# Kernel tuning notes

Measured on AMD Instinct MI355X. Metric: run time of the kernel, lower is better.

Reference implementation:

```python
import jax, jax.numpy as jnp
import numpy as np

A = 100.0
EPSILON = 0.1
NUM_NEG = 10
N = 100000
DIM = 64


def setup_inputs() -> dict:
    key = jax.random.key(0)
    k1, k2, k3 = jax.random.split(key, 3)
    x = jax.random.normal(k1, (N, DIM), dtype=jnp.float32)
    u_idx = jax.random.randint(k2, (N * NUM_NEG,), 0, N)
    v_idx = jax.random.randint(k3, (N * NUM_NEG,), 0, N)
    return {"x": x, "u_idx": u_idx, "v_idx": v_idx}


def reference(x, u_idx, v_idx):
    # Minkowski signature vector J = [-1, 1, ..., 1]
    J = jnp.ones((DIM,), dtype=x.dtype).at[0].set(-1.0)

    xu = x[u_idx]                      # (E, dim) gather
    xv = x[v_idx]                      # (E, dim) gather

    inner = jnp.sum(xu * xv * J, axis=-1)                 # (E,) Minkowski inner product
    inner = jnp.minimum(inner, -1.0 - 1e-7)               # clamp(max=-1-1e-7)
    dist = jnp.arccosh(-inner)                            # hyperbolic distance

    mask = dist < EPSILON                                 # data-dependent activity mask
    delta = jnp.where(mask, EPSILON - dist, 0.0)          # zero out inactive pairs

    energy = 0.5 * A * jnp.sum(delta ** 2) / NUM_NEG

    denom = jnp.sqrt(inner ** 2 - 1.0)
    force_mag = A * delta / NUM_NEG                       # already zero where inactive
    factor = jnp.where(mask, -(force_mag / (denom + 1e-9)), 0.0)[:, None]  # (E,1)

    grad = jnp.zeros_like(x)
    grad = grad.at[u_idx].add(factor * (xv * J))          # scatter-add over pairs
    grad = grad.at[v_idx].add(factor * (xu * J))
    return energy, grad
```

## Files before the change

### kernel.cpp

```cpp
#include <hip/hip_runtime.h>

#define EPS_F 0.1f
#define A_F 100.0f
#define NUMNEG_F 10.0f
#define EXP_EPS 1.1051709f
#define CAP 64
#define BATCH 16
#define NBLOCKS 4096

__global__ __launch_bounds__(256) void fill_kernel(
    const int* __restrict__ u_idx, const int* __restrict__ v_idx,
    int* __restrict__ counts, int* __restrict__ entries,
    float* __restrict__ out, int out_n, int E)
{
    const int tid = blockIdx.x * blockDim.x + threadIdx.x;
    const int nthreads = gridDim.x * blockDim.x;

    float4* o4 = (float4*)out;
    const int n4 = out_n >> 2;
    for (int i = tid; i < n4; i += nthreads) o4[i] = float4{0.f, 0.f, 0.f, 0.f};
    if (tid == 0)
        for (int i = n4 * 4; i < out_n; i++) out[i] = 0.f;

    for (int i = tid; i < E; i += nthreads) {
        const int u = u_idx[i];
        const int slot = atomicAdd(&counts[u], 1);
        if (slot < CAP) entries[u * CAP + slot] = v_idx[i];
    }
}

__global__ __launch_bounds__(256) void node_kernel(
    const float* __restrict__ x,
    const int* __restrict__ counts,
    const int* __restrict__ entries,
    float* __restrict__ out,
    float* __restrict__ block_energy,
    int N)
{
    const int lane = threadIdx.x & 63;
    const int wib  = threadIdx.x >> 6;
    const int wave = (blockIdx.x * blockDim.x + threadIdx.x) >> 6;
    const int nwaves = (gridDim.x * blockDim.x) >> 6;
    const float sign = (lane == 0) ? -1.0f : 1.0f;
    float* __restrict__ grad = out + 1;

    float eacc = 0.0f;

    int u = wave;
    int deg = 0, myv = 0;
    if (u < N) {
        deg = counts[u];
        myv = entries[u * CAP + lane];
    }

    while (u < N) {
        const int deg_c = min(deg, CAP);
        const int myv_c = myv;
        const float xu = x[(size_t)u * 64 + lane];

        const int un = u + nwaves;
        if (un < N) {
            deg = counts[un];
            myv = entries[un * CAP + lane];
        }

        float gacc = 0.0f;
        for (int k0 = 0; k0 < deg_c; k0 += BATCH) {
            const int bn = min(BATCH, deg_c - k0);
            int vs[BATCH]; float xv[BATCH], p[BATCH];

            #pragma unroll
            for (int k = 0; k < BATCH; k++) {
                if (k < bn) {
                    vs[k] = __builtin_amdgcn_readlane(myv_c, k0 + k);
                    xv[k] = x[(size_t)vs[k] * 64 + lane];
                }
            }
            #pragma unroll
            for (int k = 0; k < BATCH; k++)
                p[k] = (k < bn) ? xu * xv[k] * sign : 0.0f;

            #pragma unroll
            for (int off = 32; off >= 1; off >>= 1) {
                #pragma unroll
                for (int k = 0; k < BATCH; k++)
                    if (k < bn) p[k] += __shfl_xor(p[k], off, 64);
            }

            #pragma unroll
            for (int k = 0; k < BATCH; k++) {
                if (k < bn) {
                    const float inner = fminf(p[k], -1.0f - 1e-7f);
                    const float s = sqrtf(inner * inner - 1.0f);
                    const float t = -inner + s;
                    if (t < EXP_EPS) {
                        const float dist = __logf(t);
                        const float delta = EPS_F - dist;
                        eacc += delta * delta;
                        const float factor = -(A_F / NUMNEG_F) * delta / (s + 1e-9f);
                        unsafeAtomicAdd(&grad[(size_t)vs[k] * 64 + lane],
                                        factor * xu * sign);
                        gacc = fmaf(factor, xv[k], gacc);
                    }
                }
            }
        }
        if (deg_c > 0)
            unsafeAtomicAdd(&grad[(size_t)u * 64 + lane], gacc * sign);
        u = un;
    }

    __shared__ float se[4];
    if (lane == 0) se[wib] = eacc;
    __syncthreads();
    if (threadIdx.x == 0)
        block_energy[blockIdx.x] = se[0] + se[1] + se[2] + se[3];
}

__global__ __launch_bounds__(256) void energy_reduce_kernel(
    const float* __restrict__ block_energy, float* __restrict__ out, int n)
{
    const int lane = threadIdx.x & 63;
    const int wib  = threadIdx.x >> 6;
    float s = 0.0f;
    for (int i = threadIdx.x; i < n; i += 256) s += block_energy[i];
    #pragma unroll
    for (int off = 32; off >= 1; off >>= 1) s += __shfl_xor(s, off, 64);
    __shared__ float se[4];
    if (lane == 0) se[wib] = s;
    __syncthreads();
    if (threadIdx.x == 0)
        out[0] = (se[0] + se[1] + se[2] + se[3]) * (0.5f * A_F / NUMNEG_F);
}

extern "C" void kernel_launch(void* const* d_in, const int* in_sizes, int n_in,
                              void* d_out, int out_size, void* d_ws, size_t ws_size,
                              hipStream_t stream) {
    const float* x     = (const float*)d_in[0];
    const int*   u_idx = (const int*)d_in[1];
    const int*   v_idx = (const int*)d_in[2];
    float* out = (float*)d_out;
    const int E = in_sizes[1];
    const int N = in_sizes[0] / 64;

    char* ws = (char*)d_ws;
    int*   counts       = (int*)ws;
    int*   entries      = (int*)(ws + (1 << 20));
    float* block_energy = (float*)(ws + (1 << 20) + (size_t)N * CAP * 4 + (1 << 20));

    hipMemsetAsync(counts, 0, (size_t)N * sizeof(int), stream);

    fill_kernel<<<4096, 256, 0, stream>>>(u_idx, v_idx, counts, entries,
                                          out, out_size, E);

    node_kernel<<<NBLOCKS, 256, 0, stream>>>(x, counts, entries, out, block_energy, N);

    energy_reduce_kernel<<<1, 256, 0, stream>>>(block_energy, out, NBLOCKS);
}
```

Baseline: 332.1 us.

## Replace node bucketing with direct per-edge processing and transposed batched reduction

```diff
diff --git a/kernel.cpp b/kernel.cpp
--- a/kernel.cpp
+++ b/kernel.cpp
@@ -4,38 +4,22 @@
 #define A_F 100.0f
 #define NUMNEG_F 10.0f
 #define EXP_EPS 1.1051709f
-#define CAP 64
 #define BATCH 16
 #define NBLOCKS 4096
 
-__global__ __launch_bounds__(256) void fill_kernel(
-    const int* __restrict__ u_idx, const int* __restrict__ v_idx,
-    int* __restrict__ counts, int* __restrict__ entries,
-    float* __restrict__ out, int out_n, int E)
-{
-    const int tid = blockIdx.x * blockDim.x + threadIdx.x;
-    const int nthreads = gridDim.x * blockDim.x;
-
-    float4* o4 = (float4*)out;
-    const int n4 = out_n >> 2;
-    for (int i = tid; i < n4; i += nthreads) o4[i] = float4{0.f, 0.f, 0.f, 0.f};
-    if (tid == 0)
-        for (int i = n4 * 4; i < out_n; i++) out[i] = 0.f;
-
-    for (int i = tid; i < E; i += nthreads) {
-        const int u = u_idx[i];
-        const int slot = atomicAdd(&counts[u], 1);
-        if (slot < CAP) entries[u * CAP + slot] = v_idx[i];
-    }
+__device__ __forceinline__ float red2(float a, float b, int dist, bool sel) {
+    const float fa = a + __shfl_xor(a, dist, 64);
+    const float fb = b + __shfl_xor(b, dist, 64);
+    return sel ? fb : fa;
 }
 
-__global__ __launch_bounds__(256) void node_kernel(
+__global__ __launch_bounds__(256) void edge_kernel(
     const float* __restrict__ x,
-    const int* __restrict__ counts,
-    const int* __restrict__ entries,
+    const int* __restrict__ u_idx,
+    const int* __restrict__ v_idx,
     float* __restrict__ out,
     float* __restrict__ block_energy,
-    int N)
+    int E)
 {
     const int lane = threadIdx.x & 63;
     const int wib  = threadIdx.x >> 6;
@@ -44,74 +28,80 @@
     const float sign = (lane == 0) ? -1.0f : 1.0f;
     float* __restrict__ grad = out + 1;
 
+    const bool m32 = (lane & 32) != 0;
+    const bool m16 = (lane & 16) != 0;
+    const bool m8  = (lane & 8)  != 0;
+    const bool m4  = (lane & 4)  != 0;
+    const int  e4  = (lane >> 2) & 15;
+
     float eacc = 0.0f;
 
-    int u = wave;
-    int deg = 0, myv = 0;
-    if (u < N) {
-        deg = counts[u];
-        myv = entries[u * CAP + lane];
+    for (int base = wave * BATCH; base < E; base += nwaves * BATCH) {
+        const int bn = min(BATCH, E - base);
+
+        int uu = 0, vv = 0;
+        if (lane < bn) { uu = u_idx[base + lane]; vv = v_idx[base + lane]; }
+
+        int us[BATCH], vs[BATCH];
+        float xuj[BATCH], xv[BATCH];
+        #pragma unroll
+        for (int k = 0; k < BATCH; k++) {
+            if (k < bn) {
+                us[k]  = __builtin_amdgcn_readlane(uu, k);
+                vs[k]  = __builtin_amdgcn_readlane(vv, k);
+                xuj[k] = x[(size_t)us[k] * 64 + lane] * sign;
+                xv[k]  = x[(size_t)vs[k] * 64 + lane];
+            } else { us[k] = 0; vs[k] = 0; xuj[k] = 0.0f; xv[k] = 0.0f; }
+        }
+
+        float p[BATCH];
+        #pragma unroll
+        for (int k = 0; k < BATCH; k++) p[k] = xuj[k] * xv[k];
+
+        float q0 = red2(p[0], p[8],  32, m32);
+        float q1 = red2(p[1], p[9],  32, m32);
+        float q2 = red2(p[2], p[10], 32, m32);
+        float q3 = red2(p[3], p[11], 32, m32);
+        float q4 = red2(p[4], p[12], 32, m32);
+        float q5 = red2(p[5], p[13], 32, m32);
+        float q6 = red2(p[6], p[14], 32, m32);
+        float q7 = red2(p[7], p[15], 32, m32);
+        float r0 = red2(q0, q4, 16, m16);
+        float r1 = red2(q1, q5, 16, m16);
+        float r2 = red2(q2, q6, 16, m16);
+        float r3 = red2(q3, q7, 16, m16);
+        float s0 = red2(r0, r2, 8, m8);
+        float s1 = red2(r1, r3, 8, m8);
+        float t0 = red2(s0, s1, 4, m4);
+        t0 += __shfl_xor(t0, 2, 64);
+        t0 += __shfl_xor(t0, 1, 64);
+
+        const float inner = fminf(t0, -1.0f - 1e-7f);
+        const float s     = __builtin_amdgcn_sqrtf(fmaf(inner, inner, -1.0f));
+        const float t     = s - inner;
+        const bool  act   = (t < EXP_EPS) & (e4 < bn);
+        const float dist  = __logf(t);
+        const float delta = act ? (EPS_F - dist) : 0.0f;
+        eacc = fmaf(delta, delta, eacc);
+        const float factor = (-(A_F / NUMNEG_F)) * delta *
+                             __builtin_amdgcn_rcpf(s + 1e-9f);
+
+        const unsigned long long ball = __ballot(act);
+        #pragma unroll
+        for (int k = 0; k < BATCH; k++) {
+            if ((ball >> (4 * k)) & 1ull) {
+                const float fk = __uint_as_float(
+                    __builtin_amdgcn_readlane(__float_as_uint(factor), 4 * k));
+                unsafeAtomicAdd(&grad[(size_t)vs[k] * 64 + lane], fk * xuj[k]);
+                unsafeAtomicAdd(&grad[(size_t)us[k] * 64 + lane], fk * xv[k] * sign);
+            }
+        }
     }
 
-    while (u < N) {
-        const int deg_c = min(deg, CAP);
-        const int myv_c = myv;
-        const float xu = x[(size_t)u * 64 + lane];
-
-        const int un = u + nwaves;
-        if (un < N) {
-            deg = counts[un];
-            myv = entries[un * CAP + lane];
-        }
-
-        float gacc = 0.0f;
-        for (int k0 = 0; k0 < deg_c; k0 += BATCH) {
-            const int bn = min(BATCH, deg_c - k0);
-            int vs[BATCH]; float xv[BATCH], p[BATCH];
-
-            #pragma unroll
-            for (int k = 0; k < BATCH; k++) {
-                if (k < bn) {
-                    vs[k] = __builtin_amdgcn_readlane(myv_c, k0 + k);
-                    xv[k] = x[(size_t)vs[k] * 64 + lane];
-                }
-            }
-            #pragma unroll
-            for (int k = 0; k < BATCH; k++)
-                p[k] = (k < bn) ? xu * xv[k] * sign : 0.0f;
-
-            #pragma unroll
-            for (int off = 32; off >= 1; off >>= 1) {
-                #pragma unroll
-                for (int k = 0; k < BATCH; k++)
-                    if (k < bn) p[k] += __shfl_xor(p[k], off, 64);
-            }
-
-            #pragma unroll
-            for (int k = 0; k < BATCH; k++) {
-                if (k < bn) {
-                    const float inner = fminf(p[k], -1.0f - 1e-7f);
-                    const float s = sqrtf(inner * inner - 1.0f);
-                    const float t = -inner + s;
-                    if (t < EXP_EPS) {
-                        const float dist = __logf(t);
-                        const float delta = EPS_F - dist;
-                        eacc += delta * delta;
-                        const float factor = -(A_F / NUMNEG_F) * delta / (s + 1e-9f);
-                        unsafeAtomicAdd(&grad[(size_t)vs[k] * 64 + lane],
-                                        factor * xu * sign);
-                        gacc = fmaf(factor, xv[k], gacc);
-                    }
-                }
-            }
-        }
-        if (deg_c > 0)
-            unsafeAtomicAdd(&grad[(size_t)u * 64 + lane], gacc * sign);
-        u = un;
-    }
-
+    #pragma unroll
+    for (int off = 32; off >= 1; off >>= 1) eacc += __shfl_xor(eacc, off, 64);
     __shared__ float se[4];
-    if (lane == 0) se[wib] = eacc;
+    if (lane == 0) se[wib] = eacc * 0.25f;
     __syncthreads();
     if (threadIdx.x == 0)
         block_energy[blockIdx.x] = se[0] + se[1] + se[2] + se[3];
@@ -141,19 +131,10 @@
     const int*   v_idx = (const int*)d_in[2];
     float* out = (float*)d_out;
     const int E = in_sizes[1];
-    const int N = in_sizes[0] / 64;
 
-    char* ws = (char*)d_ws;
-    int*   counts       = (int*)ws;
-    int*   entries      = (int*)(ws + (1 << 20));
-    float* block_energy = (float*)(ws + (1 << 20) + (size_t)N * CAP * 4 + (1 << 20));
+    float* block_energy = (float*)d_ws;
 
-    hipMemsetAsync(counts, 0, (size_t)N * sizeof(int), stream);
-
-    fill_kernel<<<4096, 256, 0, stream>>>(u_idx, v_idx, counts, entries,
-                                          out, out_size, E);
-
-    node_kernel<<<NBLOCKS, 256, 0, stream>>>(x, counts, entries, out, block_energy, N);
-
+    hipMemsetAsync(out, 0, (size_t)out_size * sizeof(float), stream);
+    edge_kernel<<<NBLOCKS, 256, 0, stream>>>(x, u_idx, v_idx, out, block_energy, E);
     energy_reduce_kernel<<<1, 256, 0, stream>>>(block_energy, out, NBLOCKS);
 }
```

New measurement: 378.4 us. 13.9% more time.

## Use transpose-style butterfly reduction for batched dot products and lane-parallel epilogue

Applied to the files above, without the earlier changes.

```diff
diff --git a/kernel.cpp b/kernel.cpp
--- a/kernel.cpp
+++ b/kernel.cpp
@@ -29,6 +29,12 @@
     }
 }
 
+__device__ __forceinline__ float red2(float a, float b, int dist, bool sel) {
+    const float fa = a + __shfl_xor(a, dist, 64);
+    const float fb = b + __shfl_xor(b, dist, 64);
+    return sel ? fb : fa;
+}
+
 __global__ __launch_bounds__(256) void node_kernel(
     const float* __restrict__ x,
     const int* __restrict__ counts,
@@ -44,6 +50,12 @@
     const float sign = (lane == 0) ? -1.0f : 1.0f;
     float* __restrict__ grad = out + 1;
 
+    const bool m32 = (lane & 32) != 0;
+    const bool m16 = (lane & 16) != 0;
+    const bool m8  = (lane & 8)  != 0;
+    const bool m4  = (lane & 4)  != 0;
+    const int  e4  = lane >> 2;
+
     float eacc = 0.0f;
 
     int u = wave;
@@ -56,7 +68,7 @@
     while (u < N) {
         const int deg_c = min(deg, CAP);
         const int myv_c = myv;
-        const float xu = x[(size_t)u * 64 + lane];
+        const float xuj = x[(size_t)u * 64 + lane] * sign;
 
         const int un = u + nwaves;
         if (un < N) {
@@ -67,41 +79,53 @@
         float gacc = 0.0f;
         for (int k0 = 0; k0 < deg_c; k0 += BATCH) {
             const int bn = min(BATCH, deg_c - k0);
+
             int vs[BATCH]; float xv[BATCH], p[BATCH];
-
             #pragma unroll
             for (int k = 0; k < BATCH; k++) {
                 if (k < bn) {
                     vs[k] = __builtin_amdgcn_readlane(myv_c, k0 + k);
                     xv[k] = x[(size_t)vs[k] * 64 + lane];
-                }
-            }
-            #pragma unroll
-            for (int k = 0; k < BATCH; k++)
-                p[k] = (k < bn) ? xu * xv[k] * sign : 0.0f;
-
-            #pragma unroll
-            for (int off = 32; off >= 1; off >>= 1) {
-                #pragma unroll
-                for (int k = 0; k < BATCH; k++)
-                    if (k < bn) p[k] += __shfl_xor(p[k], off, 64);
+                    p[k]  = xuj * xv[k];
+                } else { vs[k] = 0; xv[k] = 0.0f; p[k] = 0.0f; }
             }
 
+            float q0 = red2(p[0], p[8],  32, m32);
+            float q1 = red2(p[1], p[9],  32, m32);
+            float q2 = red2(p[2], p[10], 32, m32);
+            float q3 = red2(p[3], p[11], 32, m32);
+            float q4 = red2(p[4], p[12], 32, m32);
+            float q5 = red2(p[5], p[13], 32, m32);
+            float q6 = red2(p[6], p[14], 32, m32);
+            float q7 = red2(p[7], p[15], 32, m32);
+            float r0 = red2(q0, q4, 16, m16);
+            float r1 = red2(q1, q5, 16, m16);
+            float r2 = red2(q2, q6, 16, m16);
+            float r3 = red2(q3, q7, 16, m16);
+            float s0 = red2(r0, r2, 8, m8);
+            float s1 = red2(r1, r3, 8, m8);
+            float t0 = red2(s0, s1, 4, m4);
+            t0 += __shfl_xor(t0, 2, 64);
+            t0 += __shfl_xor(t0, 1, 64);
+
+            const float inner = fminf(t0, -1.0f - 1e-7f);
+            const float s     = __builtin_amdgcn_sqrtf(fmaf(inner, inner, -1.0f));
+            const float t     = s - inner;
+            const bool  act   = (t < EXP_EPS) & (e4 < bn);
+            const float dist  = __logf(t);
+            const float delta = act ? (EPS_F - dist) : 0.0f;
+            eacc = fmaf(delta, delta, eacc);
+            const float factor = (-(A_F / NUMNEG_F)) * delta *
+                                 __builtin_amdgcn_rcpf(s + 1e-9f);
+
+            const unsigned long long ball = __ballot(act);
             #pragma unroll
             for (int k = 0; k < BATCH; k++) {
-                if (k < bn) {
-                    const float inner = fminf(p[k], -1.0f - 1e-7f);
-                    const float s = sqrtf(inner * inner - 1.0f);
-                    const float t = -inner + s;
-                    if (t < EXP_EPS) {
-                        const float dist = __logf(t);
-                        const float delta = EPS_F - dist;
-                        eacc += delta * delta;
-                        const float factor = -(A_F / NUMNEG_F) * delta / (s + 1e-9f);
-                        unsafeAtomicAdd(&grad[(size_t)vs[k] * 64 + lane],
-                                        factor * xu * sign);
-                        gacc = fmaf(factor, xv[k], gacc);
-                    }
+                if ((ball >> (4 * k)) & 1ull) {
+                    const float fk = __uint_as_float(
+                        __builtin_amdgcn_readlane(__float_as_uint(factor), 4 * k));
+                    unsafeAtomicAdd(&grad[(size_t)vs[k] * 64 + lane], fk * xuj);
+                    gacc = fmaf(fk, xv[k], gacc);
                 }
             }
         }
@@ -110,8 +134,10 @@
         u = un;
     }
 
+    #pragma unroll
+    for (int off = 32; off >= 1; off >>= 1) eacc += __shfl_xor(eacc, off, 64);
     __shared__ float se[4];
-    if (lane == 0) se[wib] = eacc;
+    if (lane == 0) se[wib] = eacc * 0.25f;
     __syncthreads();
     if (threadIdx.x == 0)
         block_energy[blockIdx.x] = se[0] + se[1] + se[2] + se[3];
```

Result: faster. 323.5 us (-2.6%).

## Use transposed butterfly reduction and process two nodes per wave

Applied to the files above, without the earlier changes.

```diff
diff --git a/kernel.cpp b/kernel.cpp
--- a/kernel.cpp
+++ b/kernel.cpp
@@ -25,9 +25,58 @@
     for (int i = tid; i < E; i += nthreads) {
         const int u = u_idx[i];
         const int slot = atomicAdd(&counts[u], 1);
-        if (slot < CAP) entries[u * CAP + slot] = v_idx[i];
+        if (slot < CAP) entries[(size_t)u * CAP + slot] = v_idx[i];
     }
 }
+
+__device__ __forceinline__ float red2(float a, float b, int dist, bool sel) {
+    const float fa = a + __shfl_xor(a, dist, 64);
+    const float fb = b + __shfl_xor(b, dist, 64);
+    return sel ? fb : fa;
+}
+
+#define PROCESS_BATCH(xuj, vs, xv, bn, gacc)                                   \
+    do {                                                                       \
+        float p[BATCH];                                                        \
+        _Pragma("unroll")                                                      \
+        for (int k = 0; k < BATCH; k++) p[k] = (xuj) * (xv)[k];                \
+        float q0 = red2(p[0], p[8],  32, m32);                                 \
+        float q1 = red2(p[1], p[9],  32, m32);                                 \
+        float q2 = red2(p[2], p[10], 32, m32);                                 \
+        float q3 = red2(p[3], p[11], 32, m32);                                 \
+        float q4 = red2(p[4], p[12], 32, m32);                                 \
+        float q5 = red2(p[5], p[13], 32, m32);                                 \
+        float q6 = red2(p[6], p[14], 32, m32);                                 \
+        float q7 = red2(p[7], p[15], 32, m32);                                 \
+        float r0 = red2(q0, q4, 16, m16);                                      \
+        float r1 = red2(q1, q5, 16, m16);                                      \
+        float r2 = red2(q2, q6, 16, m16);                                      \
+        float r3 = red2(q3, q7, 16, m16);                                      \
+        float s0 = red2(r0, r2, 8, m8);                                        \
+        float s1 = red2(r1, r3, 8, m8);                                        \
+        float t0 = red2(s0, s1, 4, m4);                                        \
+        t0 += __shfl_xor(t0, 2, 64);                                           \
+        t0 += __shfl_xor(t0, 1, 64);                                           \
+        const float inner = fminf(t0, -1.0f - 1e-7f);                          \
+        const float sq    = __builtin_amdgcn_sqrtf(fmaf(inner, inner, -1.0f)); \
+        const float tt    = sq - inner;                                        \
+        const bool  act   = (tt < EXP_EPS) & (e4 < (bn));                      \
+        const float dist  = __logf(tt);                                        \
+        const float delta = act ? (EPS_F - dist) : 0.0f;                       \
+        eacc = fmaf(delta, delta, eacc);                                       \
+        const float factor = (-(A_F / NUMNEG_F)) * delta *                     \
+                             __builtin_amdgcn_rcpf(sq + 1e-9f);                \
+        const unsigned long long ball = __ballot(act);                         \
+        _Pragma("unroll")                                                      \
+        for (int k = 0; k < BATCH; k++) {                                      \
+            if ((ball >> (4 * k)) & 1ull) {                                    \
+                const float fk = __uint_as_float(                              \
+                    __builtin_amdgcn_readlane(__float_as_uint(factor), 4 * k));\
+                unsafeAtomicAdd(&grad[(size_t)(vs)[k] * 64 + lane], fk * (xuj));\
+                (gacc) = fmaf(fk, (xv)[k], (gacc));                            \
+            }                                                                  \
+        }                                                                      \
+    } while (0)
 
 __global__ __launch_bounds__(256) void node_kernel(
     const float* __restrict__ x,
@@ -44,74 +93,86 @@
     const float sign = (lane == 0) ? -1.0f : 1.0f;
     float* __restrict__ grad = out + 1;
 
+    const bool m32 = (lane & 32) != 0;
+    const bool m16 = (lane & 16) != 0;
+    const bool m8  = (lane & 8)  != 0;
+    const bool m4  = (lane & 4)  != 0;
+    const int  e4  = lane >> 2;
+
     float eacc = 0.0f;
 
-    int u = wave;
-    int deg = 0, myv = 0;
-    if (u < N) {
-        deg = counts[u];
-        myv = entries[u * CAP + lane];
+    int uA = wave * 2;
+    const int stride = nwaves * 2;
+    int degA = 0, myvA = 0, degB = 0, myvB = 0;
+    if (uA < N)     { degA = counts[uA];     myvA = entries[(size_t)uA * CAP + lane]; }
+    if (uA + 1 < N) { degB = counts[uA + 1]; myvB = entries[(size_t)(uA + 1) * CAP + lane]; }
+
+    while (uA < N) {
+        const int uB = uA + 1;
+        const int bnA = min(degA, BATCH);
+        const int bnB = min(degB, BATCH);
+        const int myvA_c = myvA, myvB_c = myvB;
+
+        const float xujA = x[(size_t)uA * 64 + lane] * sign;
+        const float xujB = (uB < N) ? x[(size_t)uB * 64 + lane] * sign : 0.0f;
+
+        int vsA[BATCH], vsB[BATCH];
+        float xvA[BATCH], xvB[BATCH];
+        #pragma unroll
+        for (int k = 0; k < BATCH; k++) {
+            if (k < bnA) {
+                vsA[k] = __builtin_amdgcn_readlane(myvA_c, k);
+                xvA[k] = x[(size_t)vsA[k] * 64 + lane];
+            } else { vsA[k] = 0; xvA[k] = 0.0f; }
+        }
+        #pragma unroll
+        for (int k = 0; k < BATCH; k++) {
+            if (k < bnB) {
+                vsB[k] = __builtin_amdgcn_readlane(myvB_c, k);
+                xvB[k] = x[(size_t)vsB[k] * 64 + lane];
+            } else { vsB[k] = 0; xvB[k] = 0.0f; }
+        }
+
+        const int uAn = uA + stride;
+        int degA2 = 0, myvA2 = 0, degB2 = 0, myvB2 = 0;
+        if (uAn < N)     { degA2 = counts[uAn];     myvA2 = entries[(size_t)uAn * CAP + lane]; }
+        if (uAn + 1 < N) { degB2 = counts[uAn + 1]; myvB2 = entries[(size_t)(uAn + 1) * CAP + lane]; }
+
+        float gaccA = 0.0f, gaccB = 0.0f;
+        PROCESS_BATCH(xujA, vsA, xvA, bnA, gaccA);
+        if (bnA > 0) unsafeAtomicAdd(&grad[(size_t)uA * 64 + lane], gaccA * sign);
+        PROCESS_BATCH(xujB, vsB, xvB, bnB, gaccB);
+        if (bnB > 0) unsafeAtomicAdd(&grad[(size_t)uB * 64 + lane], gaccB * sign);
+
+        uA = uAn; degA = degA2; myvA = myvA2; degB = degB2; myvB = myvB2;
     }
 
-    while (u < N) {
+    for (int u = wave; u < N; u += nwaves) {
+        const int deg = counts[u];
+        if (deg <= BATCH) continue;
         const int deg_c = min(deg, CAP);
-        const int myv_c = myv;
-        const float xu = x[(size_t)u * 64 + lane];
-
-        const int un = u + nwaves;
-        if (un < N) {
-            deg = counts[un];
-            myv = entries[un * CAP + lane];
-        }
-
+        const int myv = entries[(size_t)u * CAP + lane];
+        const float xuj = x[(size_t)u * 64 + lane] * sign;
         float gacc = 0.0f;
-        for (int k0 = 0; k0 < deg_c; k0 += BATCH) {
+        for (int k0 = BATCH; k0 < deg_c; k0 += BATCH) {
             const int bn = min(BATCH, deg_c - k0);
-            int vs[BATCH]; float xv[BATCH], p[BATCH];
-
+            int vs[BATCH]; float xv[BATCH];
             #pragma unroll
             for (int k = 0; k < BATCH; k++) {
                 if (k < bn) {
-                    vs[k] = __builtin_amdgcn_readlane(myv_c, k0 + k);
+                    vs[k] = __builtin_amdgcn_readlane(myv, k0 + k);
                     xv[k] = x[(size_t)vs[k] * 64 + lane];
-                }
+                } else { vs[k] = 0; xv[k] = 0.0f; }
             }
-            #pragma unroll
-            for (int k = 0; k < BATCH; k++)
-                p[k] = (k < bn) ? xu * xv[k] * sign : 0.0f;
-
-            #pragma unroll
-            for (int off = 32; off >= 1; off >>= 1) {
-                #pragma unroll
-                for (int k = 0; k < BATCH; k++)
-                    if (k < bn) p[k] += __shfl_xor(p[k], off, 64);
-            }
-
-            #pragma unroll
-            for (int k = 0; k < BATCH; k++) {
-                if (k < bn) {
-                    const float inner = fminf(p[k], -1.0f - 1e-7f);
-                    const float s = sqrtf(inner * inner - 1.0f);
-                    const float t = -inner + s;
-                    if (t < EXP_EPS) {
-                        const float dist = __logf(t);
-                        const float delta = EPS_F - dist;
-                        eacc += delta * delta;
-                        const float factor = -(A_F / NUMNEG_F) * delta / (s + 1e-9f);
-                        unsafeAtomicAdd(&grad[(size_t)vs[k] * 64 + lane],
-                                        factor * xu * sign);
-                        gacc = fmaf(factor, xv[k], gacc);
-                    }
-                }
-            }
+            PROCESS_BATCH(xuj, vs, xv, bn, gacc);
         }
-        if (deg_c > 0)
-            unsafeAtomicAdd(&grad[(size_t)u * 64 + lane], gacc * sign);
-        u = un;
+        unsafeAtomicAdd(&grad[(size_t)u * 64 + lane], gacc * sign);
     }
 
+    #pragma unroll
+    for (int off = 32; off >= 1; off >>= 1) eacc += __shfl_xor(eacc, off, 64);
     __shared__ float se[4];
-    if (lane == 0) se[wib] = eacc;
+    if (lane == 0) se[wib] = eacc * 0.25f;
     __syncthreads();
     if (threadIdx.x == 0)
         block_energy[blockIdx.x] = se[0] + se[1] + se[2] + se[3];
```

Measured after the change: 314.6 us. 1.06x faster.
